# Kernel tuning notes

Hardware: AMD Instinct MI355X
Metric: run time of the kernel (lower is better)

The kernel has to match this reference:

```python
import jax, jax.numpy as jnp
import numpy as np

B, T, F = 32, 4096, 64
ALPHA = 0.9


def setup_inputs() -> dict:
    key = jax.random.key(0)
    k1, = jax.random.split(key, 1)
    spectrogram = jax.random.normal(k1, (B, T, F), dtype=jnp.float32)
    # _create_frequency_tuning: logspace(log10(1000), log10(80000), n_bands) / max
    freqs = jnp.logspace(np.log10(1000.0), np.log10(80000.0), F, dtype=jnp.float32)
    frequency_tuning = freqs / freqs.max()
    compression_threshold = jnp.float32(0.1)
    compression_ratio = jnp.float32(0.5)
    return {
        "spectrogram": spectrogram,
        "frequency_tuning": frequency_tuning,
        "compression_threshold": compression_threshold,
        "compression_ratio": compression_ratio,
    }


def reference(spectrogram, frequency_tuning, compression_threshold, compression_ratio):
    # [B, T, F] * [1, 1, F]
    tuned = spectrogram * frequency_tuning[None, None, :]
    mask = (tuned > compression_threshold).astype(tuned.dtype)
    compressed = tuned * (1.0 - mask) + (
        compression_threshold + (tuned - compression_threshold) * compression_ratio
    ) * mask
    # Leaky-integrator EMA over time: y_0 = x_0; y_t = a*y_{t-1} + (1-a)*x_t
    first = compressed[:, 0, :]                      # [B, F]
    xs = jnp.moveaxis(compressed[:, 1:, :], 1, 0)    # [T-1, B, F]

    def step(carry, x):
        y = ALPHA * carry + (1.0 - ALPHA) * x
        return y, y

    _, rest = jax.lax.scan(step, first, xs)          # [T-1, B, F]
    integrated = jnp.concatenate([first[:, None, :], jnp.moveaxis(rest, 0, 1)], axis=1)
    return jax.nn.relu(integrated)
```

## Files before the change

### kernel.cpp

```cpp
#include <hip/hip_runtime.h>


typedef float vf2 __attribute__((ext_vector_type(2)));

namespace {
constexpr int kB    = 32;
constexpr int kT    = 4096;
constexpr int kF2   = 32;
constexpr int kL    = 16;
constexpr int kSEG  = 16;
constexpr int kTBLK = kSEG * kL;
constexpr int kWALK = 2;
constexpr int kGRP  = kWALK * kTBLK;
constexpr int kNG   = kT / kGRP;
constexpr int kLW   = 4;
constexpr int kWROWS = kSEG * kLW;
constexpr float kA   = 0.9f;
constexpr float kOmA = 1.0f - kA;

constexpr float apow(int n) { float r = 1.f; for (int i = 0; i < n; ++i) r *= 0.9f; return r; }
constexpr float kA16 = apow(kL);
constexpr float kA4  = apow(kLW);
}

__global__ __launch_bounds__(kSEG * kF2, 4) void cochlea_kernel(
    const vf2* __restrict__ spec,
    const vf2* __restrict__ ftune,
    const float* __restrict__ thr_p,
    const float* __restrict__ ratio_p,
    vf2* __restrict__ out)
{
    const int tid = threadIdx.x;
    const int f2  = tid & (kF2 - 1);
    const int seg = tid >> 5;
    const int g   = blockIdx.x & (kNG - 1);
    const int b   = blockIdx.x >> 3;

    const float thr   = thr_p[0];
    const float ratio = ratio_p[0];
    const vf2 ft = ftune[f2];

    const size_t rowbase = (size_t)b * kT * kF2 + f2;
    const int tg0 = g * kGRP;

    auto comp = [&](vf2 x) -> vf2 {
        float ta = x.x * ft.x, tc = x.y * ft.y;
        float ca = fmaf(ta - thr, ratio, thr);
        float cc = fmaf(tc - thr, ratio, thr);
        vf2 v;
        v.x = (ta > thr) ? ca : ta;
        v.y = (tc > thr) ? cc : tc;
        return v;
    };

    __shared__ vf2 lds_c[kWALK][kSEG][kF2];
    __shared__ vf2 lds_w[kSEG][kF2];
    __shared__ vf2 lds_v0[kF2];

    vf2 yw = {0.f, 0.f};
    if (g > 0) {
        const vf2* wp = spec + rowbase + (size_t)(tg0 - kWROWS + seg * kLW) * kF2;
        vf2 wx[kLW];
        #pragma unroll
        for (int j = 0; j < kLW; ++j) wx[j] = wp[(size_t)j * kF2];
        #pragma unroll
        for (int j = 0; j < kLW; ++j) {
            vf2 v = comp(wx[j]);
            yw.x = fmaf(kA, yw.x, kOmA * v.x);
            yw.y = fmaf(kA, yw.y, kOmA * v.y);
        }
    }

    const vf2* sp0 = spec + rowbase + (size_t)(tg0 + seg * kL) * kF2;
    vf2 r[kL];
    vf2 y  = {0.f, 0.f};
    vf2 v0 = {0.f, 0.f};
    #pragma unroll
    for (int h = 0; h < 2; ++h) {
        vf2 xv[8];
        #pragma unroll
        for (int j = 0; j < 8; ++j) xv[j] = sp0[(size_t)(h * 8 + j) * kF2];
        #pragma unroll
        for (int j = 0; j < 8; ++j) {
            vf2 v = comp(xv[j]);
            if (h == 0 && j == 0) v0 = v;
            y.x = fmaf(kA, y.x, kOmA * v.x);
            y.y = fmaf(kA, y.y, kOmA * v.y);
            r[h * 8 + j] = y;
        }
    }
    lds_c[0][seg][f2] = y;
    lds_w[seg][f2] = yw;
    if (seg == 0) lds_v0[f2] = v0;
    __syncthreads();

    vf2 Hw;
    if (g == 0) {
        Hw = lds_v0[f2];
    } else {
        Hw = {0.f, 0.f};
        #pragma unroll
        for (int j = 0; j < kSEG; ++j) {
            vf2 w = lds_w[j][f2];
            Hw.x = fmaf(kA4, Hw.x, w.x);
            Hw.y = fmaf(kA4, Hw.y, w.y);
        }
    }

    vf2 acc = Hw, yin0 = {0.f, 0.f};
    #pragma unroll
    for (int j = 0; j < kSEG; ++j) {
        if (j == seg) yin0 = acc;
        vf2 c = lds_c[0][j][f2];
        acc.x = fmaf(kA16, acc.x, c.x);
        acc.y = fmaf(kA16, acc.y, c.y);
    }
    const vf2 I1 = acc;

    const vf2* sp1 = sp0 + (size_t)kTBLK * kF2;
    vf2 xv1[kL];
    #pragma unroll
    for (int j = 0; j < kL; ++j) xv1[j] = sp1[(size_t)j * kF2];

    vf2* op0 = out + rowbase + (size_t)(tg0 + seg * kL) * kF2;
    float ap = kA;
    #pragma unroll
    for (int j = 0; j < kL; ++j) {
        vf2 o;
        o.x = fmaxf(fmaf(ap, yin0.x, r[j].x), 0.f);
        o.y = fmaxf(fmaf(ap, yin0.y, r[j].y), 0.f);
        __builtin_nontemporal_store(o, op0 + (size_t)j * kF2);
        ap *= kA;
    }

    y = {0.f, 0.f};
    #pragma unroll
    for (int j = 0; j < kL; ++j) {
        vf2 v = comp(xv1[j]);
        y.x = fmaf(kA, y.x, kOmA * v.x);
        y.y = fmaf(kA, y.y, kOmA * v.y);
        r[j] = y;
    }
    lds_c[1][seg][f2] = y;
    __syncthreads();

    vf2 acc1 = I1, yin1 = {0.f, 0.f};
    #pragma unroll
    for (int j = 0; j < kSEG; ++j) {
        if (j == seg) yin1 = acc1;
        vf2 c = lds_c[1][j][f2];
        acc1.x = fmaf(kA16, acc1.x, c.x);
        acc1.y = fmaf(kA16, acc1.y, c.y);
    }

    vf2* op1 = op0 + (size_t)kTBLK * kF2;
    ap = kA;
    #pragma unroll
    for (int j = 0; j < kL; ++j) {
        vf2 o;
        o.x = fmaxf(fmaf(ap, yin1.x, r[j].x), 0.f);
        o.y = fmaxf(fmaf(ap, yin1.y, r[j].y), 0.f);
        __builtin_nontemporal_store(o, op1 + (size_t)j * kF2);
        ap *= kA;
    }
}

extern "C" void kernel_launch(void* const* d_in, const int* in_sizes, int n_in,
                              void* d_out, int out_size, void* d_ws, size_t ws_size,
                              hipStream_t stream) {
    const vf2*   spec  = (const vf2*)d_in[0];
    const vf2*   ftune = (const vf2*)d_in[1];
    const float* thr   = (const float*)d_in[2];
    const float* ratio = (const float*)d_in[3];
    vf2* out = (vf2*)d_out;

    dim3 grid(kB * kNG), block(kSEG * kF2);
    cochlea_kernel<<<grid, block, 0, stream>>>(spec, ftune, thr, ratio, out);
}
```

Before: 16.10 us.

## Split frequency dimension across blocks and hoist all input loads upfront

Each block now covers half of the frequency pairs (16 instead of 32), which doubles the grid to 512 blocks of 256 threads. Block indices are remapped so consecutive blocks walk across batches. All input loads (warm-up window, both time blocks) are issued at kernel start to expose more memory-level parallelism. The cost is more registers per thread (launch bounds lowered to 2) and narrower 128-byte row segments per wavefront access.

```diff
diff --git a/kernel.cpp b/kernel.cpp
--- a/kernel.cpp
+++ b/kernel.cpp
@@ -7,11 +7,11 @@
 constexpr int kB    = 32;
 constexpr int kT    = 4096;
 constexpr int kF2   = 32;
+constexpr int kFH   = 16;
 constexpr int kL    = 16;
 constexpr int kSEG  = 16;
 constexpr int kTBLK = kSEG * kL;
-constexpr int kWALK = 2;
-constexpr int kGRP  = kWALK * kTBLK;
+constexpr int kGRP  = 2 * kTBLK;
 constexpr int kNG   = kT / kGRP;
 constexpr int kLW   = 4;
 constexpr int kWROWS = kSEG * kLW;
@@ -23,7 +23,7 @@
 constexpr float kA4  = apow(kLW);
 }
 
-__global__ __launch_bounds__(kSEG * kF2, 4) void cochlea_kernel(
+__global__ __launch_bounds__(256, 2) void cochlea_kernel(
     const vf2* __restrict__ spec,
     const vf2* __restrict__ ftune,
     const float* __restrict__ thr_p,
@@ -31,16 +31,22 @@
     vf2* __restrict__ out)
 {
     const int tid = threadIdx.x;
-    const int f2  = tid & (kF2 - 1);
-    const int seg = tid >> 5;
-    const int g   = blockIdx.x & (kNG - 1);
-    const int b   = blockIdx.x >> 3;
+    const int f2  = tid & (kFH - 1);
+    const int seg = tid >> 4;
+
+    const int d    = blockIdx.x;
+    const int blo  = d & 7;
+    const int rest = d >> 3;
+    const int b    = ((rest >> 4) << 3) | blo;
+    const int sub  = rest & 15;
+    const int g    = sub >> 1;
+    const int fh   = sub & 1;
 
     const float thr   = thr_p[0];
     const float ratio = ratio_p[0];
-    const vf2 ft = ftune[f2];
+    const vf2 ft = ftune[fh * kFH + f2];
 
-    const size_t rowbase = (size_t)b * kT * kF2 + f2;
+    const size_t rowbase = (size_t)b * kT * kF2 + fh * kFH + f2;
     const int tg0 = g * kGRP;
 
     auto comp = [&](vf2 x) -> vf2 {
@@ -53,16 +59,24 @@
         return v;
     };
 
-    __shared__ vf2 lds_c[kWALK][kSEG][kF2];
-    __shared__ vf2 lds_w[kSEG][kF2];
-    __shared__ vf2 lds_v0[kF2];
+    const vf2* sp0 = spec + rowbase + (size_t)(tg0 + seg * kL) * kF2;
+    const vf2* sp1 = sp0 + (size_t)kTBLK * kF2;
+
+    vf2 wx[kLW];
+    if (g > 0) {
+        const vf2* wp = spec + rowbase + (size_t)(tg0 - kWROWS + seg * kLW) * kF2;
+        #pragma unroll
+        for (int j = 0; j < kLW; ++j) wx[j] = wp[(size_t)j * kF2];
+    }
+    vf2 xv0[kL];
+    #pragma unroll
+    for (int j = 0; j < kL; ++j) xv0[j] = sp0[(size_t)j * kF2];
+    vf2 xv1[kL];
+    #pragma unroll
+    for (int j = 0; j < kL; ++j) xv1[j] = sp1[(size_t)j * kF2];
 
     vf2 yw = {0.f, 0.f};
     if (g > 0) {
-        const vf2* wp = spec + rowbase + (size_t)(tg0 - kWROWS + seg * kLW) * kF2;
-        vf2 wx[kLW];
-        #pragma unroll
-        for (int j = 0; j < kLW; ++j) wx[j] = wp[(size_t)j * kF2];
         #pragma unroll
         for (int j = 0; j < kLW; ++j) {
             vf2 v = comp(wx[j]);
@@ -71,24 +85,21 @@
         }
     }
 
-    const vf2* sp0 = spec + rowbase + (size_t)(tg0 + seg * kL) * kF2;
     vf2 r[kL];
     vf2 y  = {0.f, 0.f};
     vf2 v0 = {0.f, 0.f};
     #pragma unroll
-    for (int h = 0; h < 2; ++h) {
-        vf2 xv[8];
-        #pragma unroll
-        for (int j = 0; j < 8; ++j) xv[j] = sp0[(size_t)(h * 8 + j) * kF2];
-        #pragma unroll
-        for (int j = 0; j < 8; ++j) {
-            vf2 v = comp(xv[j]);
-            if (h == 0 && j == 0) v0 = v;
-            y.x = fmaf(kA, y.x, kOmA * v.x);
-            y.y = fmaf(kA, y.y, kOmA * v.y);
-            r[h * 8 + j] = y;
-        }
+    for (int j = 0; j < kL; ++j) {
+        vf2 v = comp(xv0[j]);
+        if (j == 0) v0 = v;
+        y.x = fmaf(kA, y.x, kOmA * v.x);
+        y.y = fmaf(kA, y.y, kOmA * v.y);
+        r[j] = y;
     }
+
+    __shared__ vf2 lds_c[2][kSEG][kFH];
+    __shared__ vf2 lds_w[kSEG][kFH];
+    __shared__ vf2 lds_v0[kFH];
     lds_c[0][seg][f2] = y;
     lds_w[seg][f2] = yw;
     if (seg == 0) lds_v0[f2] = v0;
@@ -116,11 +127,6 @@
         acc.y = fmaf(kA16, acc.y, c.y);
     }
     const vf2 I1 = acc;
-
-    const vf2* sp1 = sp0 + (size_t)kTBLK * kF2;
-    vf2 xv1[kL];
-    #pragma unroll
-    for (int j = 0; j < kL; ++j) xv1[j] = sp1[(size_t)j * kF2];
 
     vf2* op0 = out + rowbase + (size_t)(tg0 + seg * kL) * kF2;
     float ap = kA;
@@ -174,6 +180,6 @@
     const float* ratio = (const float*)d_in[3];
     vf2* out = (vf2*)d_out;
 
-    dim3 grid(kB * kNG), block(kSEG * kF2);
+    dim3 grid(kB * kNG * 2), block(kSEG * kFH);
     cochlea_kernel<<<grid, block, 0, stream>>>(spec, ftune, thr, ratio, out);
 }
```

Measured after the change: 13.60 us (median of 2 runs). 1.18x faster.
